# Kernel tuning notes

Hardware: AMD Instinct MI355X
Metric: run time of the kernel (lower is better)

Reference implementation:

```python
import jax, jax.numpy as jnp
import numpy as np

S = 14       # grid size
B = 2        # boxes per cell
C = 20       # classes
N_EL = B * 5 + C   # 30
L_COORD = 5.0
L_NOOBJ = 0.5
BATCH = 4096
NBOX = 16


def setup_inputs() -> dict:
    key = jax.random.key(0)
    k1, k2, k3, k4 = jax.random.split(key, 4)
    prediction = jax.random.uniform(k1, (BATCH, S * S * N_EL), dtype=jnp.float32)
    # well-formed ground-truth boxes: centers in (0.05,0.95), sizes in (0.02,0.3)
    cxcy = jax.random.uniform(k2, (BATCH, NBOX, 2), minval=0.05, maxval=0.95, dtype=jnp.float32)
    wh = jax.random.uniform(k3, (BATCH, NBOX, 2), minval=0.02, maxval=0.3, dtype=jnp.float32)
    boxes = jnp.concatenate([cxcy - wh / 2, cxcy + wh / 2], axis=-1)  # x1,y1,x2,y2
    classes = jax.random.randint(k4, (BATCH, NBOX), 0, C, dtype=jnp.int32)
    return {"prediction": prediction, "boxes": boxes, "classes": classes}


def _encode(boxes, classes):
    """Vectorized version of YoloLoss.encode: scatter boxes into SxS grid cells.
    Faithful detail: class one-hot goes to channel 9+class (the original's
    off-by-one: class 0 lands on the 2nd confidence channel)."""
    bsz, nbox = classes.shape
    cell = 1.0 / S
    xy1, xy2 = boxes[..., :2], boxes[..., 2:]
    wh = xy2 - xy1
    cxcy = (xy1 + xy2) / 2
    ij = jnp.clip(jnp.ceil(cxcy / cell) - 1, 0, S - 1)          # [b,nbox,2] (x,y)
    dxy = cxcy / cell - ij                                      # delta inside cell
    ij = ij.astype(jnp.int32)
    one = jnp.ones_like(wh[..., :1])
    zcls = jnp.zeros(classes.shape + (C,), dtype=boxes.dtype)
    # layout: [dxy, wh, conf, dxy, wh, conf, class one-hots]
    base = jnp.concatenate([dxy, wh, one, dxy, wh, one, zcls], axis=-1)  # [b,nbox,30]
    cls_oh = jax.nn.one_hot(classes + (B * 5 - 1), N_EL, dtype=boxes.dtype)  # index 9+class
    vec = jnp.maximum(base, cls_oh)
    flat_idx = (jnp.arange(bsz, dtype=jnp.int32)[:, None] * (S * S)
                + ij[..., 1] * S + ij[..., 0]).reshape(-1)      # row-major (y,x)
    target = jnp.zeros((bsz * S * S, N_EL), dtype=boxes.dtype)
    return target.at[flat_idx].set(vec.reshape(-1, N_EL))


def _pairwise_iou(a, b):
    """a,b: [N,B,4] -> iou [N,B(pred),B(target)] (corner-format jaccard, as in
    the original, applied to (dx,dy,w,h) rows verbatim)."""
    a4 = a[:, :, None, :]
    b4 = b[:, None, :, :]
    lt = jnp.maximum(a4[..., :2], b4[..., :2])
    rb = jnp.minimum(a4[..., 2:], b4[..., 2:])
    whi = jnp.clip(rb - lt, 0.0)
    inter = whi[..., 0] * whi[..., 1]
    area_a = (a4[..., 2] - a4[..., 0]) * (a4[..., 3] - a4[..., 1])
    area_b = (b4[..., 2] - b4[..., 0]) * (b4[..., 3] - b4[..., 1])
    union = area_a + area_b - inter
    return inter / jnp.where(union == 0, 1.0, union)


def reference(prediction, boxes, classes):
    target = _encode(boxes, classes)                       # [bsz*S*S, 30]
    pred = prediction.reshape(-1, N_EL)
    coord = target[:, 4] > 0                               # cells containing objects
    coordf = coord.astype(pred.dtype)
    noobjf = (target[:, 4] == 0).astype(pred.dtype)

    conf_idx = jnp.array([4, 9])
    noobj_loss = jnp.sum(noobjf[:, None] * (pred[:, conf_idx] - target[:, conf_idx]) ** 2)
    class_loss = jnp.sum(coordf[:, None] * (pred[:, B * 5:] - target[:, B * 5:]) ** 2)

    bp = pred[:, :B * 5].reshape(-1, B, 5)                 # [N,B,5]
    bt = target[:, :B * 5].reshape(-1, B, 5)

    iou = _pairwise_iou(bp[..., :4], bt[..., :4])          # [N,B,B]
    max_index = jnp.argmax(iou, axis=1)                    # best pred per target box
    response = (max_index[:, None, :] == jnp.arange(B)[None, :, None]).any(-1)  # [N,B]
    resp = response & coord[:, None]
    respf = resp.astype(pred.dtype)

    contain_loss = jnp.sum(respf * (bp[..., 4] - bt[..., 4]) ** 2)
    bt_wh = jnp.where(resp[..., None], bt[..., 2:4], 1.0)  # guard sqrt at masked cells
    loc_loss = jnp.sum(respf * (((bp[..., :2] - bt[..., :2]) ** 2).sum(-1)
                                + ((jnp.sqrt(bp[..., 2:4]) - jnp.sqrt(bt_wh)) ** 2).sum(-1)))

    return L_COORD * loc_loss + contain_loss + L_NOOBJ * noobj_loss + class_loss
```

## Files before the change

### kernel.cpp

```cpp
#include <hip/hip_runtime.h>


#define SGRID 14
#define CELLS 196
#define NEL 30
#define NBOX 16
#define PRED_PER_BATCH (CELLS * NEL)

__global__ void encode_kernel(const float* __restrict__ boxes,
                              const int*   __restrict__ classes,
                              int*   __restrict__ winner,
                              float* __restrict__ params,
                              int nbb)
{
    int t = blockIdx.x * blockDim.x + threadIdx.x;
    if (t >= nbb) return;
    int b = t >> 4;
    int k = t & 15;
    float4 bx = ((const float4*)boxes)[t];
    float w  = bx.z - bx.x,  h  = bx.w - bx.y;
    float cx = (bx.x + bx.z) * 0.5f, cy = (bx.y + bx.w) * 0.5f;
    const float cellw = (float)(1.0 / 14.0);
    float fx = cx / cellw, fy = cy / cellw;
    float fi = fminf(fmaxf(ceilf(fx) - 1.0f, 0.0f), 13.0f);
    float fj = fminf(fmaxf(ceilf(fy) - 1.0f, 0.0f), 13.0f);
    int cell = (int)fj * SGRID + (int)fi;
    float* pr = params + (size_t)t * 8;
    pr[0] = fx - fi;  pr[1] = fy - fj;
    pr[2] = w;        pr[3] = h;
    pr[4] = (float)classes[t];
    atomicMax(&winner[b * CELLS + cell], k);
}

__global__ __launch_bounds__(256) void yolo_main_kernel(
    const float* __restrict__ pred,
    const int*   __restrict__ winner,
    const float* __restrict__ params,
    float* __restrict__ partials,
    int total)
{
    int idx = blockIdx.x * 256 + threadIdx.x;
    float loss = 0.0f;
    if (idx < total) {
        int b    = idx / CELLS;
        const float* p = pred + (size_t)idx * NEL;
        int k = winner[idx];
        if (k < 0) {
            float2 a = *(const float2*)(p + 4);
            float2 c = *(const float2*)(p + 8);
            loss = 0.5f * (a.x * a.x + c.y * c.y);
        } else {
            float pp[NEL];
            #pragma unroll
            for (int j = 0; j < NEL / 2; ++j)
                ((float2*)pp)[j] = ((const float2*)p)[j];
            const float* pr = params + (size_t)(b * NBOX + k) * 8;
            float dx = pr[0], dy = pr[1], w = pr[2], h = pr[3];
            int cls = (int)pr[4];

            int hot = 9 + cls;
            #pragma unroll
            for (int c = 10; c < NEL; ++c) {
                float t = (c == hot) ? 1.0f : 0.0f;
                float d = pp[c] - t;
                loss += d * d;
            }

            float area_t = (w - dx) * (h - dy);
            float iou[2];
            #pragma unroll
            for (int i = 0; i < 2; ++i) {
                const float* a = pp + i * 5;
                float ltx = fmaxf(a[0], dx), lty = fmaxf(a[1], dy);
                float rbx = fminf(a[2], w),  rby = fminf(a[3], h);
                float wi = fmaxf(rbx - ltx, 0.0f);
                float hi = fmaxf(rby - lty, 0.0f);
                float inter  = wi * hi;
                float area_a = (a[2] - a[0]) * (a[3] - a[1]);
                float uni    = area_a + area_t - inter;
                iou[i] = inter / ((uni == 0.0f) ? 1.0f : uni);
            }
            int r = (iou[1] > iou[0]) ? 1 : 0;
            const float* a = pp + r * 5;

            float dc = a[4] - 1.0f;
            loss += dc * dc;
            float lx = a[0] - dx;
            float ly = a[1] - dy;
            float lw = sqrtf(a[2]) - sqrtf(w);
            float lh = sqrtf(a[3]) - sqrtf(h);
            loss += 5.0f * (lx * lx + ly * ly + lw * lw + lh * lh);
        }
    }

    #pragma unroll
    for (int off = 32; off > 0; off >>= 1)
        loss += __shfl_down(loss, off, 64);
    if ((threadIdx.x & 63) == 0)
        partials[(blockIdx.x * 256 + threadIdx.x) >> 6] = loss;
}

__global__ __launch_bounds__(256) void reduce_kernel(
    const float* __restrict__ partials, float* __restrict__ out, int n)
{
    float s = 0.0f;
    for (int i = threadIdx.x; i < n; i += 256) s += partials[i];
    #pragma unroll
    for (int off = 32; off > 0; off >>= 1)
        s += __shfl_down(s, off, 64);
    __shared__ float w4[4];
    if ((threadIdx.x & 63) == 0) w4[threadIdx.x >> 6] = s;
    __syncthreads();
    if (threadIdx.x == 0) out[0] = w4[0] + w4[1] + w4[2] + w4[3];
}

extern "C" void kernel_launch(void* const* d_in, const int* in_sizes, int n_in,
                              void* d_out, int out_size, void* d_ws, size_t ws_size,
                              hipStream_t stream) {
    const float* pred    = (const float*)d_in[0];
    const float* boxes   = (const float*)d_in[1];
    const int*   classes = (const int*)d_in[2];
    float* out = (float*)d_out;

    const int batch = in_sizes[0] / PRED_PER_BATCH;
    const int total = batch * CELLS;
    const int nbb   = batch * NBOX;

    int*   winner   = (int*)d_ws;
    float* params   = (float*)((char*)d_ws + (size_t)total * sizeof(int));
    float* partials = params + (size_t)nbb * 8;
    const int mgrid  = (total + 255) / 256;
    const int nwaves = mgrid * 4;

    hipMemsetAsync(winner, 0xFF, (size_t)total * sizeof(int), stream);
    encode_kernel<<<dim3((nbb + 255) / 256), dim3(256), 0, stream>>>(
        boxes, classes, winner, params, nbb);
    yolo_main_kernel<<<dim3(mgrid), dim3(256), 0, stream>>>(
        pred, winner, params, partials, total);
    reduce_kernel<<<dim3(1), dim3(256), 0, stream>>>(partials, out, nwaves);
}
```

Baseline: 159.1 us.

## Split loss into coalesced float4 stream pass and per-box object pass

Replaces the per-cell main kernel, which made strided 120-byte reads per thread, with a stream kernel that reads the prediction tensor as contiguous float4 vectors. Each element gets its noobj-confidence or class term from the cell's winner word, which now packs the box index and hot class channel. A separate per-box kernel recomputes the box encoding and evaluates IoU, responsible-box, coordinate and confidence losses only for winning boxes, dropping the params buffer. This costs two winner lookups and an integer divide per vector, one extra kernel launch, and rereads the first ten floats of occupied cells.

```diff
diff --git a/kernel.cpp b/kernel.cpp
--- a/kernel.cpp
+++ b/kernel.cpp
@@ -5,102 +5,128 @@
 #define CELLS 196
 #define NEL 30
 #define NBOX 16
-#define PRED_PER_BATCH (CELLS * NEL)
+#define PRED_PER_BATCH 5880
+#define STREAM_ITERS 12
+#define STREAM_TPB 256
+#define STREAM_CHUNK (STREAM_ITERS * STREAM_TPB)
 
-__global__ void encode_kernel(const float* __restrict__ boxes,
-                              const int*   __restrict__ classes,
-                              int*   __restrict__ winner,
-                              float* __restrict__ params,
-                              int nbb)
+__device__ __forceinline__ void block_reduce_store(float v, float* slot) {
+    #pragma unroll
+    for (int off = 32; off > 0; off >>= 1)
+        v += __shfl_down(v, off, 64);
+    __shared__ float w4[4];
+    int tid = threadIdx.x;
+    if ((tid & 63) == 0) w4[tid >> 6] = v;
+    __syncthreads();
+    if (tid == 0) *slot = w4[0] + w4[1] + w4[2] + w4[3];
+}
+
+__global__ __launch_bounds__(256) void encode_kernel(
+    const float4* __restrict__ boxes, const int* __restrict__ classes,
+    int* __restrict__ winner, int nbb)
 {
-    int t = blockIdx.x * blockDim.x + threadIdx.x;
+    int t = blockIdx.x * 256 + threadIdx.x;
     if (t >= nbb) return;
-    int b = t >> 4;
-    int k = t & 15;
-    float4 bx = ((const float4*)boxes)[t];
-    float w  = bx.z - bx.x,  h  = bx.w - bx.y;
+    int b = t >> 4, k = t & 15;
+    float4 bx = boxes[t];
+    const float cellw = (float)(1.0 / 14.0);
     float cx = (bx.x + bx.z) * 0.5f, cy = (bx.y + bx.w) * 0.5f;
-    const float cellw = (float)(1.0 / 14.0);
     float fx = cx / cellw, fy = cy / cellw;
     float fi = fminf(fmaxf(ceilf(fx) - 1.0f, 0.0f), 13.0f);
     float fj = fminf(fmaxf(ceilf(fy) - 1.0f, 0.0f), 13.0f);
     int cell = (int)fj * SGRID + (int)fi;
-    float* pr = params + (size_t)t * 8;
-    pr[0] = fx - fi;  pr[1] = fy - fj;
-    pr[2] = w;        pr[3] = h;
-    pr[4] = (float)classes[t];
-    atomicMax(&winner[b * CELLS + cell], k);
+    int hot = 9 + classes[t];
+    atomicMax(&winner[b * CELLS + cell], (k << 8) | hot);
 }
 
-__global__ __launch_bounds__(256) void yolo_main_kernel(
-    const float* __restrict__ pred,
-    const int*   __restrict__ winner,
-    const float* __restrict__ params,
-    float* __restrict__ partials,
-    int total)
+__global__ __launch_bounds__(256) void stream_kernel(
+    const float4* __restrict__ pred4, const int* __restrict__ winner,
+    float* __restrict__ partials, int nvec)
 {
-    int idx = blockIdx.x * 256 + threadIdx.x;
+    int base = blockIdx.x * STREAM_CHUNK + threadIdx.x;
     float loss = 0.0f;
-    if (idx < total) {
-        int b    = idx / CELLS;
-        const float* p = pred + (size_t)idx * NEL;
-        int k = winner[idx];
-        if (k < 0) {
-            float2 a = *(const float2*)(p + 4);
-            float2 c = *(const float2*)(p + 8);
-            loss = 0.5f * (a.x * a.x + c.y * c.y);
-        } else {
-            float pp[NEL];
+    #pragma unroll
+    for (int i = 0; i < STREAM_ITERS; ++i) {
+        int e = base + i * STREAM_TPB;
+        if (e < nvec) {
+            float4 v = pred4[e];
+            int g = e * 4;
+            int cell = (int)((unsigned)g / 30u);
+            int c0 = g - cell * 30;
+            int m0 = winner[cell];
+            int m1 = winner[cell + 1];
+            float pv[4] = {v.x, v.y, v.z, v.w};
             #pragma unroll
-            for (int j = 0; j < NEL / 2; ++j)
-                ((float2*)pp)[j] = ((const float2*)p)[j];
-            const float* pr = params + (size_t)(b * NBOX + k) * 8;
-            float dx = pr[0], dy = pr[1], w = pr[2], h = pr[3];
-            int cls = (int)pr[4];
+            for (int j = 0; j < 4; ++j) {
+                int cj = c0 + j;
+                int cc = (cj >= 30) ? cj - 30 : cj;
+                int m  = (cj >= 30) ? m1 : m0;
+                bool isconf = (cc == 4) | (cc == 9);
+                float wgt = isconf ? ((m < 0) ? 0.5f : 0.0f)
+                                   : ((cc >= 10) ? ((m >= 0) ? 1.0f : 0.0f) : 0.0f);
+                float tt = (cc == (m & 0xFF)) ? 1.0f : 0.0f;
+                float d = pv[j] - tt;
+                loss += wgt * d * d;
+            }
+        }
+    }
+    block_reduce_store(loss, &partials[blockIdx.x]);
+}
 
-            int hot = 9 + cls;
+__global__ __launch_bounds__(256) void obj_kernel(
+    const float* __restrict__ pred, const float4* __restrict__ boxes,
+    const int* __restrict__ winner, float* __restrict__ partials, int nbb)
+{
+    int t = blockIdx.x * 256 + threadIdx.x;
+    float loss = 0.0f;
+    if (t < nbb) {
+        int b = t >> 4, k = t & 15;
+        float4 bx = boxes[t];
+        const float cellw = (float)(1.0 / 14.0);
+        float w = bx.z - bx.x, h = bx.w - bx.y;
+        float cx = (bx.x + bx.z) * 0.5f, cy = (bx.y + bx.w) * 0.5f;
+        float fx = cx / cellw, fy = cy / cellw;
+        float fi = fminf(fmaxf(ceilf(fx) - 1.0f, 0.0f), 13.0f);
+        float fj = fminf(fmaxf(ceilf(fy) - 1.0f, 0.0f), 13.0f);
+        float dx = fx - fi, dy = fy - fj;
+        int idx = b * CELLS + (int)fj * SGRID + (int)fi;
+        int wv = winner[idx];
+        if ((wv >> 8) == k) {
+            const float* p = pred + (size_t)idx * NEL;
+            float a[10];
             #pragma unroll
-            for (int c = 10; c < NEL; ++c) {
-                float t = (c == hot) ? 1.0f : 0.0f;
-                float d = pp[c] - t;
-                loss += d * d;
+            for (int j = 0; j < 5; ++j) {
+                float2 v = *(const float2*)(p + 2 * j);
+                a[2 * j] = v.x;  a[2 * j + 1] = v.y;
             }
-
             float area_t = (w - dx) * (h - dy);
             float iou[2];
             #pragma unroll
             for (int i = 0; i < 2; ++i) {
-                const float* a = pp + i * 5;
-                float ltx = fmaxf(a[0], dx), lty = fmaxf(a[1], dy);
-                float rbx = fminf(a[2], w),  rby = fminf(a[3], h);
+                const float* q = a + i * 5;
+                float ltx = fmaxf(q[0], dx), lty = fmaxf(q[1], dy);
+                float rbx = fminf(q[2], w),  rby = fminf(q[3], h);
                 float wi = fmaxf(rbx - ltx, 0.0f);
                 float hi = fmaxf(rby - lty, 0.0f);
                 float inter  = wi * hi;
-                float area_a = (a[2] - a[0]) * (a[3] - a[1]);
+                float area_a = (q[2] - q[0]) * (q[3] - q[1]);
                 float uni    = area_a + area_t - inter;
                 iou[i] = inter / ((uni == 0.0f) ? 1.0f : uni);
             }
             int r = (iou[1] > iou[0]) ? 1 : 0;
-            const float* a = pp + r * 5;
-
-            float dc = a[4] - 1.0f;
+            const float* q = a + r * 5;
+            float dc = q[4] - 1.0f;
             loss += dc * dc;
-            float lx = a[0] - dx;
-            float ly = a[1] - dy;
-            float lw = sqrtf(a[2]) - sqrtf(w);
-            float lh = sqrtf(a[3]) - sqrtf(h);
+            float lx = q[0] - dx, ly = q[1] - dy;
+            float lw = sqrtf(q[2]) - sqrtf(w);
+            float lh = sqrtf(q[3]) - sqrtf(h);
             loss += 5.0f * (lx * lx + ly * ly + lw * lw + lh * lh);
         }
     }
-
-    #pragma unroll
-    for (int off = 32; off > 0; off >>= 1)
-        loss += __shfl_down(loss, off, 64);
-    if ((threadIdx.x & 63) == 0)
-        partials[(blockIdx.x * 256 + threadIdx.x) >> 6] = loss;
+    block_reduce_store(loss, &partials[blockIdx.x]);
 }
 
-__global__ __launch_bounds__(256) void reduce_kernel(
+__global__ __launch_bounds__(256) void final_reduce_kernel(
     const float* __restrict__ partials, float* __restrict__ out, int n)
 {
     float s = 0.0f;
@@ -125,17 +151,21 @@
     const int batch = in_sizes[0] / PRED_PER_BATCH;
     const int total = batch * CELLS;
     const int nbb   = batch * NBOX;
+    const int nvec  = total * NEL / 4;
+
+    const int sblocks = (nvec + STREAM_CHUNK - 1) / STREAM_CHUNK;
+    const int oblocks = (nbb + 255) / 256;
+    const int nparts  = sblocks + oblocks;
 
     int*   winner   = (int*)d_ws;
-    float* params   = (float*)((char*)d_ws + (size_t)total * sizeof(int));
-    float* partials = params + (size_t)nbb * 8;
-    const int mgrid  = (total + 255) / 256;
-    const int nwaves = mgrid * 4;
+    float* partials = (float*)((char*)d_ws + (size_t)(total + 1) * sizeof(int));
 
-    hipMemsetAsync(winner, 0xFF, (size_t)total * sizeof(int), stream);
+    hipMemsetAsync(winner, 0xFF, (size_t)(total + 1) * sizeof(int), stream);
     encode_kernel<<<dim3((nbb + 255) / 256), dim3(256), 0, stream>>>(
-        boxes, classes, winner, params, nbb);
-    yolo_main_kernel<<<dim3(mgrid), dim3(256), 0, stream>>>(
-        pred, winner, params, partials, total);
-    reduce_kernel<<<dim3(1), dim3(256), 0, stream>>>(partials, out, nwaves);
+        (const float4*)boxes, classes, winner, nbb);
+    stream_kernel<<<dim3(sblocks), dim3(256), 0, stream>>>(
+        (const float4*)pred, winner, partials, nvec);
+    obj_kernel<<<dim3(oblocks), dim3(256), 0, stream>>>(
+        pred, (const float4*)boxes, winner, partials + sblocks, nbb);
+    final_reduce_kernel<<<dim3(1), dim3(256), 0, stream>>>(partials, out, nparts);
 }
```

New measurement: 159.4 us. Within noise of the previous version (+0.2%).
